# Kernel tuning notes

Hardware: AMD Instinct MI355X
Metric: run time of the kernel (lower is better)

Reference implementation:

```python
import jax, jax.numpy as jnp
import numpy as np

B, NPG, DEG = 128, 400, 16
N, E = B * NPG, B * NPG * DEG
E_PER = E // B
K1, K2, K3 = 360, 324, 292  # ceil(0.9*400), ceil(0.9*360), ceil(0.9*324)
EPS = 1e-5


def setup_inputs() -> dict:
    key = jax.random.key(0)
    ks = jax.random.split(key, 48)
    # edges constrained within each graph (contiguous equal-size graphs)
    g = jnp.repeat(jnp.arange(B, dtype=jnp.int32), E_PER)
    src = jax.random.randint(ks[0], (E,), 0, NPG, dtype=jnp.int32) + g * NPG
    dst = jax.random.randint(ks[1], (E,), 0, NPG, dtype=jnp.int32) + g * NPG
    inp = {
        'x': jax.random.normal(ks[2], (N, 64), dtype=jnp.float32),
        'edge_index': jnp.stack([src, dst]),
        'batch': jnp.repeat(jnp.arange(B, dtype=jnp.int32), NPG),
    }
    def glorot(k, a, b):
        lim = float(np.sqrt(6.0 / (a + b)))
        return jax.random.uniform(k, (a, b), minval=-lim, maxval=lim, dtype=jnp.float32)
    conv_dims = [(64, 32), (32, 64), (64, 128), (128, 128)]
    for i, (a, b) in enumerate(conv_dims, 1):
        inp[f'W{i}'] = glorot(ks[2 + i], a, b)
        inp[f'b{i}'] = jnp.zeros((b,), jnp.float32)
    for i, d in zip((1, 2, 3), (32, 64, 128)):
        inp[f'p{i}'] = jax.random.uniform(ks[8 + i], (d,), minval=-1.0, maxval=1.0, dtype=jnp.float32) / float(np.sqrt(d))
    lin_dims = [(128, 64), (64, 64), (64, 32), (32, 16), (16, 1)]
    for i, (a, b) in enumerate(lin_dims, 1):
        inp[f'Lw{i}'] = glorot(ks[12 + i], a, b)
        inp[f'Lb{i}'] = jnp.zeros((b,), jnp.float32)
    for i, d in enumerate((64, 64, 32, 16), 1):
        inp[f'g{i}'] = jnp.ones((d,), jnp.float32)
        inp[f'be{i}'] = jnp.zeros((d,), jnp.float32)
    return inp


def _gcn(x, src, dst, emask, nmask, W, b):
    h = x @ W
    deg = nmask + jax.ops.segment_sum(emask, dst, num_segments=N)
    dinv = jnp.where(deg > 0, jax.lax.rsqrt(deg), 0.0)
    norm = dinv[src] * dinv[dst] * emask
    agg = jax.ops.segment_sum(h[src] * norm[:, None], dst, num_segments=N)
    agg = agg + h * (dinv * dinv * nmask)[:, None]  # self-loop term
    return (agg + b) * nmask[:, None]


def _topk_pool(x, nmask, p, k):
    # PyG TopKPooling: score = x.p/||p||, keep top-k per graph, x *= tanh(score)
    score = (x @ p) / jnp.linalg.norm(p)
    sel = jnp.where(nmask > 0, score, -jnp.inf).reshape(B, NPG)
    _, idx = jax.lax.top_k(sel, k)
    gidx = (idx + (jnp.arange(B) * NPG)[:, None]).reshape(-1)
    new_mask = jnp.zeros((N,), x.dtype).at[gidx].set(1.0)
    return x * (jnp.tanh(score) * new_mask)[:, None], new_mask


def reference(x, edge_index, batch, W1, b1, p1, W2, b2, p2, W3, b3, p3, W4, b4,
              Lw1, Lb1, Lw2, Lb2, Lw3, Lb3, Lw4, Lb4, Lw5, Lb5,
              g1, be1, g2, be2, g3, be3, g4, be4):
    src, dst = edge_index[0], edge_index[1]
    nmask = jnp.ones((N,), jnp.float32)
    emask = jnp.ones((E,), jnp.float32)
    x = jax.nn.relu(_gcn(x, src, dst, emask, nmask, W1, b1))
    x, nmask = _topk_pool(x, nmask, p1, K1)
    emask = emask * nmask[src] * nmask[dst]
    x = jax.nn.relu(_gcn(x, src, dst, emask, nmask, W2, b2))
    x, nmask = _topk_pool(x, nmask, p2, K2)
    emask = emask * nmask[src] * nmask[dst]
    x = jax.nn.relu(_gcn(x, src, dst, emask, nmask, W3, b3))
    x, nmask = _topk_pool(x, nmask, p3, K3)
    emask = emask * nmask[src] * nmask[dst]
    x = jax.nn.relu(_gcn(x, src, dst, emask, nmask, W4, b4))
    h = x.reshape(B, NPG, -1).max(axis=1)
    def lin_bn(h, W, bb, ga, be):
        h = h @ W + bb
        m = h.mean(0)
        v = h.var(0)  # biased, matches BatchNorm1d training normalization
        return jax.nn.relu(ga * (h - m) / jnp.sqrt(v + EPS) + be)
    h = lin_bn(h, Lw1, Lb1, g1, be1)
    h = lin_bn(h, Lw2, Lb2, g2, be2)
    h = lin_bn(h, Lw3, Lb3, g3, be3)
    h = lin_bn(h, Lw4, Lb4, g4, be4)
    return h @ Lw5 + Lb5
```

## Files before the change

kernel.cpp:

```cpp
#include <hip/hip_runtime.h>
#include <math.h>

#define NNODES 51200
#define BGRAPHS 128
#define NPG 400
#define NEDGES 819200
#define EPG 6400
#define SLP 7680

__device__ __forceinline__ float4 ld4(const float* p) { return *reinterpret_cast<const float4*>(p); }
__device__ __forceinline__ void st4(float* p, float4 v) { *reinterpret_cast<float4*>(p) = v; }

__global__ __launch_bounds__(512) void csr_build_kernel(
    const int* __restrict__ src, const int* __restrict__ dst,
    unsigned short* __restrict__ slg, int* __restrict__ gsg, int* __restrict__ gcg,
    float* __restrict__ nmask, float* __restrict__ dinv, float* __restrict__ sc,
    float* __restrict__ hp) {
    __shared__ int deg[NPG];
    __shared__ int incl[512];
    __shared__ int gs[NPG];
    __shared__ int cur[NPG];
    const int g = blockIdx.x, t = threadIdx.x;
    for (int i = t; i < NPG; i += 512) deg[i] = 0;
    if (t < 128) hp[g * 128 + t] = 0.0f;
    __syncthreads();
    for (int e = t; e < EPG; e += 512)
        atomicAdd(&deg[dst[g * EPG + e] - g * NPG], 1);
    __syncthreads();
    const int d = (t < NPG) ? deg[t] : 0;
    const int p = (d + 3) >> 2;
    incl[t] = p;
    __syncthreads();
    for (int off = 1; off < 512; off <<= 1) {
        int add = (t >= off) ? incl[t - off] : 0;
        __syncthreads();
        incl[t] += add;
        __syncthreads();
    }
    if (t < NPG) {
        const int gstart = incl[t] - p;
        gs[t] = gstart;
        gsg[g * NPG + t] = gstart;
        gcg[g * NPG + t] = p;
        cur[t] = gstart * 4;
        nmask[g * NPG + t] = 1.0f;
        const float dv = rsqrtf(1.0f + (float)d);
        dinv[g * NPG + t] = dv;
        sc[g * NPG + t] = dv;
    }
    __syncthreads();
    for (int e = t; e < EPG; e += 512) {
        int dl = dst[g * EPG + e] - g * NPG;
        int pos = atomicAdd(&cur[dl], 1);
        slg[g * SLP + pos] = (unsigned short)(src[g * EPG + e] - g * NPG);
    }
    __syncthreads();
    if (t < NPG) {
        const int end = (gs[t] + p) * 4;
        for (int i = cur[t]; i < end; i++) slg[g * SLP + i] = (unsigned short)NPG;
    }
}

template<int IN, int OUT, int MODE>
__global__ __launch_bounds__(256) void gemm_kernel(
    const float* __restrict__ X, const float* __restrict__ W,
    const float* __restrict__ bias, const float* __restrict__ nmask,
    float* __restrict__ H, const float* __restrict__ p,
    float* __restrict__ score, float* __restrict__ hp) {
    __shared__ __align__(16) float sX[64 * IN];
    __shared__ unsigned smax[256];
    const int row0 = blockIdx.x * 64;
    const int t = threadIdx.x;
    for (int i = t; i < 64 * IN / 4; i += 256)
        reinterpret_cast<float4*>(sX)[i] =
            reinterpret_cast<const float4*>(X + (size_t)row0 * IN)[i];
    if (MODE == 3) smax[t] = 0u;
    __syncthreads();
    constexpr int CG  = OUT / 4;
    constexpr int RG  = 256 / CG;
    constexpr int RPT = 64 / RG;
    const int c0 = (t % CG) * 4;
    const int r0 = (t / CG) * RPT;
    float acc[RPT][4];
#pragma unroll
    for (int r = 0; r < RPT; r++)
#pragma unroll
        for (int j = 0; j < 4; j++) acc[r][j] = 0.0f;
    for (int k4 = 0; k4 < IN / 4; k4++) {
        const float4 w0 = ld4(&W[(k4 * 4 + 0) * OUT + c0]);
        const float4 w1 = ld4(&W[(k4 * 4 + 1) * OUT + c0]);
        const float4 w2 = ld4(&W[(k4 * 4 + 2) * OUT + c0]);
        const float4 w3 = ld4(&W[(k4 * 4 + 3) * OUT + c0]);
#pragma unroll
        for (int r = 0; r < RPT; r++) {
            const float4 xv = ld4(&sX[(r0 + r) * IN + k4 * 4]);
            acc[r][0] += xv.x * w0.x + xv.y * w1.x + xv.z * w2.x + xv.w * w3.x;
            acc[r][1] += xv.x * w0.y + xv.y * w1.y + xv.z * w2.y + xv.w * w3.y;
            acc[r][2] += xv.x * w0.z + xv.y * w1.z + xv.z * w2.z + xv.w * w3.z;
            acc[r][3] += xv.x * w0.w + xv.y * w1.w + xv.z * w2.w + xv.w * w3.w;
        }
    }
    const int graph0 = row0 / 400;
    const int bnd = (graph0 + 1) * 400;
    float ps[RPT];
    float cmax[4] = {0.f, 0.f, 0.f, 0.f};
#pragma unroll
    for (int r = 0; r < RPT; r++) {
        const int row = row0 + r0 + r;
        float4 v = make_float4(acc[r][0], acc[r][1], acc[r][2], acc[r][3]);
        if (MODE >= 2) {
            const float4 b4 = ld4(&bias[c0]);
            const float m = nmask[row];
            v.x = fmaxf(v.x + b4.x, 0.0f) * m;
            v.y = fmaxf(v.y + b4.y, 0.0f) * m;
            v.z = fmaxf(v.z + b4.z, 0.0f) * m;
            v.w = fmaxf(v.w + b4.w, 0.0f) * m;
        }
        if (MODE != 3) st4(&H[(size_t)row * OUT + c0], v);
        if (MODE == 2) {
            const float4 p4 = ld4(&p[c0]);
            ps[r] = v.x * p4.x + v.y * p4.y + v.z * p4.z + v.w * p4.w;
        }
        if (MODE == 3) {
            cmax[0] = fmaxf(cmax[0], v.x);
            cmax[1] = fmaxf(cmax[1], v.y);
            cmax[2] = fmaxf(cmax[2], v.z);
            cmax[3] = fmaxf(cmax[3], v.w);
        }
    }
    if (MODE == 2) {
#pragma unroll
        for (int r = 0; r < RPT; r++) {
#pragma unroll
            for (int off = 1; off < CG; off <<= 1) ps[r] += __shfl_xor(ps[r], off);
        }
        if ((t % CG) == 0) {
#pragma unroll
            for (int r = 0; r < RPT; r++) score[row0 + r0 + r] = ps[r];
        }
    }
    if (MODE == 3) {
        const int seg = ((row0 + r0) >= bnd) ? 1 : 0;
        atomicMax(&smax[seg * 128 + c0 + 0], __float_as_uint(cmax[0]));
        atomicMax(&smax[seg * 128 + c0 + 1], __float_as_uint(cmax[1]));
        atomicMax(&smax[seg * 128 + c0 + 2], __float_as_uint(cmax[2]));
        atomicMax(&smax[seg * 128 + c0 + 3], __float_as_uint(cmax[3]));
        __syncthreads();
        unsigned* hpu = reinterpret_cast<unsigned*>(hp);
        if (t < 128) atomicMax(&hpu[graph0 * 128 + t], smax[t]);
        const int graph1 = (row0 + 63) / 400;
        if (graph1 != graph0 && t < 128) atomicMax(&hpu[graph1 * 128 + t], smax[128 + t]);
    }
}

template<int OUT, int NCH, int NS, bool EPI, bool SCORE, bool TOPK>
__global__ __launch_bounds__(512) void gcn_agg_kernel(
    const float* __restrict__ H, float* __restrict__ Y,
    const float* __restrict__ dinv_g, const float* __restrict__ sc_g,
    const float* __restrict__ bias,
    const float* __restrict__ p_sc, float* __restrict__ score_out,
    const float* __restrict__ scoreb_in, const float* __restrict__ nmask_in,
    float* __restrict__ nmask_out, const float* __restrict__ p_pool,
    int K, int PDIM,
    const unsigned short* __restrict__ slg, const int* __restrict__ gsg,
    const int* __restrict__ gcg) {
    __shared__ __align__(16) float Hl[(NPG + 1) * 36];
    __shared__ float dinvl[NPG];
    __shared__ float scl[NPG];
    __shared__ int gsl[NPG];
    __shared__ int gcl[NPG];
    __shared__ unsigned long long sl64[SLP / 4];
    __shared__ float misc[4];
    const unsigned short* sl = reinterpret_cast<const unsigned short*>(sl64);
    const int b   = blockIdx.x;
    const int g   = b / (NCH * NS);
    const int rem = b % (NCH * NS);
    const int f0  = (rem / NS) * 32;
    const int n0  = (rem % NS) * (NPG / NS);
    const int t   = threadIdx.x;

    for (int i = t; i < NPG; i += 512) {
        gsl[i] = gsg[g * NPG + i];
        gcl[i] = gcg[g * NPG + i];
    }
    for (int i = t; i < SLP / 4; i += 512)
        sl64[i] = reinterpret_cast<const unsigned long long*>(slg + (size_t)g * SLP)[i];

    if (TOPK) {
        float* sval = Hl;
        int*   sidx = (int*)(Hl + 512);
        float* sraw = Hl + 1024;
        float* nml  = Hl + 1440;
        if (t < 64) {
            float s = 0.0f;
            for (int j = t; j < PDIM; j += 64) s += p_pool[j] * p_pool[j];
#pragma unroll
            for (int o = 32; o > 0; o >>= 1) s += __shfl_xor(s, o, 64);
            if (t == 0) misc[0] = sqrtf(s);
        }
        float v = -INFINITY;
        int ix = t;
        if (t < NPG) {
            const float raw = scoreb_in[g * NPG + t];
            sraw[t] = raw;
            v = (nmask_in[g * NPG + t] > 0.0f) ? raw : -INFINITY;
        }
        __syncthreads();
        for (int kk = 2; kk <= 512; kk <<= 1) {
            for (int j = kk >> 1; j > 0; j >>= 1) {
                float vb; int ib;
                if (j >= 64) {
                    sval[t] = v; sidx[t] = ix;
                    __syncthreads();
                    vb = sval[t ^ j]; ib = sidx[t ^ j];
                    __syncthreads();
                } else {
                    vb = __shfl_xor(v, j, 64);
                    ib = __shfl_xor(ix, j, 64);
                }
                const bool ownFirst = (v > vb) || (v == vb && ix < ib);
                const bool lower = (t & j) == 0;
                const bool desc = (t & kk) == 0;
                const bool keepOwn = lower ? (desc == ownFirst) : (desc != ownFirst);
                if (!keepOwn) { v = vb; ix = ib; }
            }
        }
        if (t <= NPG) nml[t] = 0.0f;
        __syncthreads();
        if (t < K) nml[ix] = 1.0f;
        __syncthreads();
        if (rem == 0 && t < NPG) nmask_out[g * NPG + t] = nml[t];
        const float spn = misc[0];
        for (int n = t; n < NPG; n += 512) {
            float dv = 0.0f;
            if (nml[n] > 0.0f) {
                float d = 1.0f;
                const int g0 = gsl[n], g1 = g0 + gcl[n];
                for (int gg = g0; gg < g1; ++gg) {
                    const unsigned long long q = *reinterpret_cast<const unsigned long long*>(&sl[gg * 4]);
                    d += nml[(int)(q & 0xFFFF)] + nml[(int)((q >> 16) & 0xFFFF)] +
                         nml[(int)((q >> 32) & 0xFFFF)] + nml[(int)(q >> 48)];
                }
                dv = rsqrtf(d);
            }
            dinvl[n] = dv;
            scl[n] = (nml[n] > 0.0f) ? tanhf(sraw[n] / spn) * dv : 0.0f;
        }
        __syncthreads();
    } else {
        for (int i = t; i < NPG; i += 512) {
            dinvl[i] = dinv_g[g * NPG + i];
            scl[i]   = sc_g[g * NPG + i];
        }
        __syncthreads();
    }

    for (int i = t; i < NPG * 8; i += 512) {
        const int n = i >> 3, q = i & 7;
        const float s = scl[n];
        float4 v = ld4(&H[(size_t)(g * NPG + n) * OUT + f0 + q * 4]);
        v.x *= s; v.y *= s; v.z *= s; v.w *= s;
        st4(&Hl[n * 36 + q * 4], v);
    }
    if (t < 36) Hl[NPG * 36 + t] = 0.0f;
    __syncthreads();

    const int wave = t >> 6, lane = t & 63;
    const int sub = lane >> 3, f4 = lane & 7;
    constexpr int NPB = NPG / NS;
    for (int n = n0 + wave * 8 + sub; n < n0 + NPB; n += 64) {
        const float di = dinvl[n];
        if (di == 0.0f) continue;
        const int g0 = gsl[n], g1 = g0 + gcl[n];
        float4 acc = ld4(&Hl[n * 36 + f4 * 4]);
        for (int gg = g0; gg < g1; ++gg) {
            const unsigned long long q = *reinterpret_cast<const unsigned long long*>(&sl[gg * 4]);
            const int s0 = (int)(q & 0xFFFF), s1 = (int)((q >> 16) & 0xFFFF);
            const int s2 = (int)((q >> 32) & 0xFFFF), s3 = (int)(q >> 48);
            const float4 a = ld4(&Hl[s0 * 36 + f4 * 4]);
            const float4 bb = ld4(&Hl[s1 * 36 + f4 * 4]);
            const float4 c = ld4(&Hl[s2 * 36 + f4 * 4]);
            const float4 dd = ld4(&Hl[s3 * 36 + f4 * 4]);
            acc.x += (a.x + bb.x) + (c.x + dd.x);
            acc.y += (a.y + bb.y) + (c.y + dd.y);
            acc.z += (a.z + bb.z) + (c.z + dd.z);
            acc.w += (a.w + bb.w) + (c.w + dd.w);
        }
        acc.x *= di; acc.y *= di; acc.z *= di; acc.w *= di;
        if (EPI) {
            const float4 b4 = ld4(&bias[f0 + f4 * 4]);
            acc.x = fmaxf(acc.x + b4.x, 0.0f);
            acc.y = fmaxf(acc.y + b4.y, 0.0f);
            acc.z = fmaxf(acc.z + b4.z, 0.0f);
            acc.w = fmaxf(acc.w + b4.w, 0.0f);
        }
        st4(&Y[(size_t)(g * NPG + n) * OUT + f0 + f4 * 4], acc);
        if (SCORE) {
            const float4 p4 = ld4(&p_sc[f4 * 4]);
            float part = acc.x * p4.x + acc.y * p4.y + acc.z * p4.z + acc.w * p4.w;
            part += __shfl_xor(part, 1);
            part += __shfl_xor(part, 2);
            part += __shfl_xor(part, 4);
            if (f4 == 0) score_out[g * NPG + n] = part;
        }
    }
}

__global__ __launch_bounds__(512) void conv2_fused_kernel(
    const float* __restrict__ X0, float* __restrict__ X1,
    const float* __restrict__ scoreb_in, const float* __restrict__ nmask_in,
    float* __restrict__ nmask_out, float* __restrict__ scoreb_out,
    const float* __restrict__ p_pool,
    const float* __restrict__ W2, const float* __restrict__ b2,
    const float* __restrict__ p2,
    const unsigned short* __restrict__ slg, const int* __restrict__ gsg,
    const int* __restrict__ gcg) {
    __shared__ __align__(16) float Hl[(NPG + 1) * 36];
    __shared__ __align__(16) float out2[200 * 36];
    __shared__ float dinvl[NPG];
    __shared__ float scl[NPG];
    __shared__ int gsl[NPG];
    __shared__ int gcl[NPG];
    __shared__ unsigned long long sl64[SLP / 4];
    __shared__ float misc[4];
    const unsigned short* sl = reinterpret_cast<const unsigned short*>(sl64);
    const int b = blockIdx.x, g = b >> 1, seg = b & 1;
    const int n0 = seg * 200;
    const int t = threadIdx.x;

    for (int i = t; i < NPG; i += 512) {
        gsl[i] = gsg[g * NPG + i];
        gcl[i] = gcg[g * NPG + i];
    }
    for (int i = t; i < SLP / 4; i += 512)
        sl64[i] = reinterpret_cast<const unsigned long long*>(slg + (size_t)g * SLP)[i];

    {
        float* sval = Hl;
        int*   sidx = (int*)(Hl + 512);
        float* sraw = Hl + 1024;
        float* nml  = Hl + 1440;
        if (t < 64) {
            float s = 0.0f;
            for (int j = t; j < 32; j += 64) s += p_pool[j] * p_pool[j];
#pragma unroll
            for (int o = 32; o > 0; o >>= 1) s += __shfl_xor(s, o, 64);
            if (t == 0) misc[0] = sqrtf(s);
        }
        float v = -INFINITY;
        int ix = t;
        if (t < NPG) {
            const float raw = scoreb_in[g * NPG + t];
            sraw[t] = raw;
            v = (nmask_in[g * NPG + t] > 0.0f) ? raw : -INFINITY;
        }
        __syncthreads();
        for (int kk = 2; kk <= 512; kk <<= 1) {
            for (int j = kk >> 1; j > 0; j >>= 1) {
                float vb; int ib;
                if (j >= 64) {
                    sval[t] = v; sidx[t] = ix;
                    __syncthreads();
                    vb = sval[t ^ j]; ib = sidx[t ^ j];
                    __syncthreads();
                } else {
                    vb = __shfl_xor(v, j, 64);
                    ib = __shfl_xor(ix, j, 64);
                }
                const bool ownFirst = (v > vb) || (v == vb && ix < ib);
                const bool lower = (t & j) == 0;
                const bool desc = (t & kk) == 0;
                const bool keepOwn = lower ? (desc == ownFirst) : (desc != ownFirst);
                if (!keepOwn) { v = vb; ix = ib; }
            }
        }
        if (t <= NPG) nml[t] = 0.0f;
        __syncthreads();
        if (t < 360) nml[ix] = 1.0f;
        __syncthreads();
        if (seg == 0 && t < NPG) nmask_out[g * NPG + t] = nml[t];
        const float spn = misc[0];
        for (int n = t; n < NPG; n += 512) {
            float dv = 0.0f;
            if (nml[n] > 0.0f) {
                float d = 1.0f;
                const int g0 = gsl[n], g1 = g0 + gcl[n];
                for (int gg = g0; gg < g1; ++gg) {
                    const unsigned long long q = *reinterpret_cast<const unsigned long long*>(&sl[gg * 4]);
                    d += nml[(int)(q & 0xFFFF)] + nml[(int)((q >> 16) & 0xFFFF)] +
                         nml[(int)((q >> 32) & 0xFFFF)] + nml[(int)(q >> 48)];
                }
                dv = rsqrtf(d);
            }
            dinvl[n] = dv;
            scl[n] = (nml[n] > 0.0f) ? tanhf(sraw[n] / spn) * dv : 0.0f;
        }
        __syncthreads();
    }

    for (int i = t; i < NPG * 8; i += 512) {
        const int n = i >> 3, q = i & 7;
        const float s = scl[n];
        float4 v = ld4(&X0[(size_t)(g * NPG + n) * 32 + q * 4]);
        v.x *= s; v.y *= s; v.z *= s; v.w *= s;
        st4(&Hl[n * 36 + q * 4], v);
    }
    if (t < 36) Hl[NPG * 36 + t] = 0.0f;
    __syncthreads();

    {
        const int wave = t >> 6, lane = t & 63;
        const int sub = lane >> 3, f4 = lane & 7;
        for (int n = n0 + wave * 8 + sub; n < n0 + 200; n += 64) {
            const float di = dinvl[n];
            float4 acc = make_float4(0.f, 0.f, 0.f, 0.f);
            if (di != 0.0f) {
                acc = ld4(&Hl[n * 36 + f4 * 4]);
                const int g0 = gsl[n], g1 = g0 + gcl[n];
                for (int gg = g0; gg < g1; ++gg) {
                    const unsigned long long q = *reinterpret_cast<const unsigned long long*>(&sl[gg * 4]);
                    const int s0 = (int)(q & 0xFFFF), s1 = (int)((q >> 16) & 0xFFFF);
                    const int s2 = (int)((q >> 32) & 0xFFFF), s3 = (int)(q >> 48);
                    const float4 a = ld4(&Hl[s0 * 36 + f4 * 4]);
                    const float4 bb = ld4(&Hl[s1 * 36 + f4 * 4]);
                    const float4 c = ld4(&Hl[s2 * 36 + f4 * 4]);
                    const float4 dd = ld4(&Hl[s3 * 36 + f4 * 4]);
                    acc.x += (a.x + bb.x) + (c.x + dd.x);
                    acc.y += (a.y + bb.y) + (c.y + dd.y);
                    acc.z += (a.z + bb.z) + (c.z + dd.z);
                    acc.w += (a.w + bb.w) + (c.w + dd.w);
                }
                acc.x *= di; acc.y *= di; acc.z *= di; acc.w *= di;
            }
            st4(&out2[(n - n0) * 36 + f4 * 4], acc);
        }
    }
    __syncthreads();

    {
        const int c0 = (t & 15) * 4;
        const int slot = t >> 4;
        for (int n = n0 + slot; n < n0 + 200; n += 32) {
            float a0 = 0.f, a1 = 0.f, a2 = 0.f, a3 = 0.f;
            for (int k4 = 0; k4 < 8; k4++) {
                const float4 w0 = ld4(&W2[(k4 * 4 + 0) * 64 + c0]);
                const float4 w1 = ld4(&W2[(k4 * 4 + 1) * 64 + c0]);
                const float4 w2 = ld4(&W2[(k4 * 4 + 2) * 64 + c0]);
                const float4 w3 = ld4(&W2[(k4 * 4 + 3) * 64 + c0]);
                const float4 xv = ld4(&out2[(n - n0) * 36 + k4 * 4]);
                a0 += xv.x * w0.x + xv.y * w1.x + xv.z * w2.x + xv.w * w3.x;
                a1 += xv.x * w0.y + xv.y * w1.y + xv.z * w2.y + xv.w * w3.y;
                a2 += xv.x * w0.z + xv.y * w1.z + xv.z * w2.z + xv.w * w3.z;
                a3 += xv.x * w0.w + xv.y * w1.w + xv.z * w2.w + xv.w * w3.w;
            }
            const float m = (dinvl[n] > 0.0f) ? 1.0f : 0.0f;
            const float4 bb = ld4(&b2[c0]);
            float4 v = make_float4(fmaxf(a0 + bb.x, 0.f) * m, fmaxf(a1 + bb.y, 0.f) * m,
                                   fmaxf(a2 + bb.z, 0.f) * m, fmaxf(a3 + bb.w, 0.f) * m);
            st4(&X1[(size_t)(g * NPG + n) * 64 + c0], v);
            const float4 p4 = ld4(&p2[c0]);
            float ps = v.x * p4.x + v.y * p4.y + v.z * p4.z + v.w * p4.w;
            ps += __shfl_xor(ps, 1); ps += __shfl_xor(ps, 2);
            ps += __shfl_xor(ps, 4); ps += __shfl_xor(ps, 8);
            if ((t & 15) == 0) scoreb_out[g * NPG + n] = ps;
        }
    }
}

template<int IN, int OUT>
__global__ __launch_bounds__(128) void head_layer_kernel(
    const float* __restrict__ A, const float* __restrict__ W,
    const float* __restrict__ b, const float* __restrict__ ga,
    const float* __restrict__ be, float* __restrict__ Y) {
    __shared__ float Al[128 * (IN + 1)];
    __shared__ float red[4];
    const int c = blockIdx.x, t = threadIdx.x;
    for (int i = t; i < 128 * IN; i += 128)
        Al[(i / IN) * (IN + 1) + (i % IN)] = A[i];
    __syncthreads();
    float acc = b[c];
#pragma unroll
    for (int j = 0; j < IN; j++) acc += Al[t * (IN + 1) + j] * W[j * OUT + c];
    float s1 = acc, s2 = acc * acc;
    for (int o = 32; o > 0; o >>= 1) {
        s1 += __shfl_down(s1, o, 64);
        s2 += __shfl_down(s2, o, 64);
    }
    if ((t & 63) == 0) { red[t >> 6] = s1; red[2 + (t >> 6)] = s2; }
    __syncthreads();
    const float S1 = red[0] + red[1], S2 = red[2] + red[3];
    const float m = S1 * (1.0f / 128.0f);
    const float var = S2 * (1.0f / 128.0f) - m * m;
    float val = ga[c] * (acc - m) * rsqrtf(var + 1e-5f) + be[c];
    Y[t * OUT + c] = fmaxf(val, 0.0f);
}

__global__ __launch_bounds__(512) void head_tail_kernel(
    const float* __restrict__ A2,
    const float* __restrict__ Lw3, const float* __restrict__ Lb3,
    const float* __restrict__ g3, const float* __restrict__ be3,
    const float* __restrict__ Lw4, const float* __restrict__ Lb4,
    const float* __restrict__ g4, const float* __restrict__ be4,
    const float* __restrict__ Lw5, const float* __restrict__ Lb5,
    float* __restrict__ out) {
    __shared__ __align__(16) float A[128 * 68];
    __shared__ __align__(16) float Z[128 * 36];
    __shared__ __align__(16) float Z2[128 * 20];
    __shared__ float mv[64];
    const int t = threadIdx.x;
    for (int i = t; i < 128 * 16; i += 512) {
        const int r = i >> 4, q = i & 15;
        st4(&A[r * 68 + q * 4], ld4(&A2[r * 64 + q * 4]));
    }
    __syncthreads();
    {
        const int c = t & 31, rs = t >> 5;
        for (int r = rs; r < 128; r += 16) {
            float acc = Lb3[c];
            for (int j4 = 0; j4 < 16; j4++) {
                const float4 a = ld4(&A[r * 68 + j4 * 4]);
                acc += a.x * Lw3[(j4 * 4 + 0) * 32 + c] + a.y * Lw3[(j4 * 4 + 1) * 32 + c]
                     + a.z * Lw3[(j4 * 4 + 2) * 32 + c] + a.w * Lw3[(j4 * 4 + 3) * 32 + c];
            }
            Z[r * 36 + c] = acc;
        }
    }
    __syncthreads();
    if (t < 32) {
        float s1 = 0.f, s2 = 0.f;
        for (int r = 0; r < 128; r++) { const float v = Z[r * 36 + t]; s1 += v; s2 += v * v; }
        const float m = s1 * (1.0f / 128.0f);
        mv[t] = m; mv[32 + t] = s2 * (1.0f / 128.0f) - m * m;
    }
    __syncthreads();
    {
        const int c = t & 31;
        const float m = mv[c], scn = g3[c] * rsqrtf(mv[32 + c] + 1e-5f), bb = be3[c];
        for (int r = t >> 5; r < 128; r += 16)
            Z[r * 36 + c] = fmaxf((Z[r * 36 + c] - m) * scn + bb, 0.f);
    }
    __syncthreads();
    {
        const int c = t & 15, rs = t >> 4;
        for (int r = rs; r < 128; r += 32) {
            float acc = Lb4[c];
            for (int j4 = 0; j4 < 8; j4++) {
                const float4 a = ld4(&Z[r * 36 + j4 * 4]);
                acc += a.x * Lw4[(j4 * 4 + 0) * 16 + c] + a.y * Lw4[(j4 * 4 + 1) * 16 + c]
                     + a.z * Lw4[(j4 * 4 + 2) * 16 + c] + a.w * Lw4[(j4 * 4 + 3) * 16 + c];
            }
            Z2[r * 20 + c] = acc;
        }
    }
    __syncthreads();
    if (t < 16) {
        float s1 = 0.f, s2 = 0.f;
        for (int r = 0; r < 128; r++) { const float v = Z2[r * 20 + t]; s1 += v; s2 += v * v; }
        const float m = s1 * (1.0f / 128.0f);
        mv[t] = m; mv[32 + t] = s2 * (1.0f / 128.0f) - m * m;
    }
    __syncthreads();
    if (t < 128) {
        float acc = Lb5[0];
#pragma unroll
        for (int j = 0; j < 16; j++) {
            const float v = fmaxf((Z2[t * 20 + j] - mv[j]) * (g4[j] * rsqrtf(mv[32 + j] + 1e-5f)) + be4[j], 0.f);
            acc += v * Lw5[j];
        }
        out[t] = acc;
    }
}

extern "C" void kernel_launch(void* const* d_in, const int* in_sizes, int n_in,
                              void* d_out, int out_size, void* d_ws, size_t ws_size,
                              hipStream_t stream) {
    (void)in_sizes; (void)n_in; (void)out_size; (void)ws_size;
    const float* x   = (const float*)d_in[0];
    const int*   ei  = (const int*)d_in[1];
    const float* W1  = (const float*)d_in[3];  const float* b1  = (const float*)d_in[4];
    const float* W2  = (const float*)d_in[5];  const float* b2  = (const float*)d_in[6];
    const float* W3  = (const float*)d_in[7];  const float* b3  = (const float*)d_in[8];
    const float* W4  = (const float*)d_in[9];  const float* b4  = (const float*)d_in[10];
    const float* p1  = (const float*)d_in[11];
    const float* p2  = (const float*)d_in[12];
    const float* p3  = (const float*)d_in[13];
    const float* Lw1 = (const float*)d_in[14]; const float* Lb1 = (const float*)d_in[15];
    const float* Lw2 = (const float*)d_in[16]; const float* Lb2 = (const float*)d_in[17];
    const float* Lw3 = (const float*)d_in[18]; const float* Lb3 = (const float*)d_in[19];
    const float* Lw4 = (const float*)d_in[20]; const float* Lb4 = (const float*)d_in[21];
    const float* Lw5 = (const float*)d_in[22]; const float* Lb5 = (const float*)d_in[23];
    const float* g1  = (const float*)d_in[24]; const float* be1 = (const float*)d_in[25];
    const float* g2  = (const float*)d_in[26]; const float* be2 = (const float*)d_in[27];
    const float* g3  = (const float*)d_in[28]; const float* be3 = (const float*)d_in[29];
    const float* g4  = (const float*)d_in[30]; const float* be4 = (const float*)d_in[31];

    const int* src = ei;
    const int* dst = ei + NEDGES;

    float* ws    = (float*)d_ws;
    float* hb    = ws;
    float* x0    = hb + (size_t)NNODES * 128;
    float* x1    = x0 + (size_t)NNODES * 128;
    float* nmA   = x1 + (size_t)NNODES * 128;
    float* nmB   = nmA + NNODES;
    float* dinv  = nmB + NNODES;
    float* sc    = dinv + NNODES;
    float* scbA  = sc + NNODES;
    float* scbB  = scbA + NNODES;
    float* hp    = scbB + NNODES;
    float* a1    = hp + 128 * 128;
    float* a2    = a1 + 128 * 64;
    unsigned short* slg = (unsigned short*)(a2 + 128 * 64);
    int* gsg = (int*)(slg + (size_t)BGRAPHS * SLP);
    int* gcg = gsg + (size_t)BGRAPHS * NPG;

    csr_build_kernel<<<BGRAPHS, 512, 0, stream>>>(src, dst, slg, gsg, gcg, nmA, dinv, sc, hp);

    gemm_kernel<64, 32, 0><<<NNODES / 64, 256, 0, stream>>>(x, W1, nullptr, nullptr, hb, nullptr, nullptr, nullptr);
    gcn_agg_kernel<32, 1, 2, true, true, false><<<BGRAPHS * 2, 512, 0, stream>>>(
        hb, x0, dinv, sc, b1, p1, scbA,
        nullptr, nullptr, nullptr, nullptr, 0, 0, slg, gsg, gcg);

    conv2_fused_kernel<<<BGRAPHS * 2, 512, 0, stream>>>(
        x0, x1, scbA, nmA, nmB, scbB, p1, W2, b2, p2, slg, gsg, gcg);

    gcn_agg_kernel<64, 2, 2, false, false, true><<<BGRAPHS * 4, 512, 0, stream>>>(
        x1, hb, nullptr, nullptr, nullptr, nullptr, nullptr,
        scbB, nmB, nmA, p2, 324, 64, slg, gsg, gcg);
    gemm_kernel<64, 128, 2><<<NNODES / 64, 256, 0, stream>>>(hb, W3, b3, nmA, x0, p3, scbA, nullptr);

    gcn_agg_kernel<128, 4, 1, false, false, true><<<BGRAPHS * 4, 512, 0, stream>>>(
        x0, hb, nullptr, nullptr, nullptr, nullptr, nullptr,
        scbA, nmA, nmB, p3, 292, 128, slg, gsg, gcg);
    gemm_kernel<128, 128, 3><<<NNODES / 64, 256, 0, stream>>>(hb, W4, b4, nmB, x1, nullptr, nullptr, hp);

    head_layer_kernel<128, 64><<<64, 128, 0, stream>>>(hp, Lw1, Lb1, g1, be1, a1);
    head_layer_kernel<64, 64><<<64, 128, 0, stream>>>(a1, Lw2, Lb2, g2, be2, a2);
    head_tail_kernel<<<1, 512, 0, stream>>>(a2, Lw3, Lb3, g3, be3, Lw4, Lb4, g4, be4, Lw5, Lb5, (float*)d_out);
}
```

Baseline: 192.4 us.

## Fuse CSR build and first GEMM into one heterogeneous kernel launch

The CSR construction kernel and the first 64->32 projection GEMM are merged into one launch. The first 128 blocks build per-graph adjacency and the remaining 256 blocks run the GEMM over 128-row tiles, so the two independent phases run concurrently and one launch is dropped. Because MODE 0 is no longer used, the gemm template's bias/relu/mask epilogue is made unconditional. The cost is a larger shared allocation for every block and an uneven block workload.

```diff
diff --git a/kernel.cpp b/kernel.cpp
--- a/kernel.cpp
+++ b/kernel.cpp
@@ -11,53 +11,94 @@
 __device__ __forceinline__ float4 ld4(const float* p) { return *reinterpret_cast<const float4*>(p); }
 __device__ __forceinline__ void st4(float* p, float4 v) { *reinterpret_cast<float4*>(p) = v; }
 
-__global__ __launch_bounds__(512) void csr_build_kernel(
+__global__ __launch_bounds__(512) void csr_gemm1_kernel(
     const int* __restrict__ src, const int* __restrict__ dst,
     unsigned short* __restrict__ slg, int* __restrict__ gsg, int* __restrict__ gcg,
     float* __restrict__ nmask, float* __restrict__ dinv, float* __restrict__ sc,
-    float* __restrict__ hp) {
-    __shared__ int deg[NPG];
-    __shared__ int incl[512];
-    __shared__ int gs[NPG];
-    __shared__ int cur[NPG];
-    const int g = blockIdx.x, t = threadIdx.x;
-    for (int i = t; i < NPG; i += 512) deg[i] = 0;
-    if (t < 128) hp[g * 128 + t] = 0.0f;
-    __syncthreads();
-    for (int e = t; e < EPG; e += 512)
-        atomicAdd(&deg[dst[g * EPG + e] - g * NPG], 1);
-    __syncthreads();
-    const int d = (t < NPG) ? deg[t] : 0;
-    const int p = (d + 3) >> 2;
-    incl[t] = p;
-    __syncthreads();
-    for (int off = 1; off < 512; off <<= 1) {
-        int add = (t >= off) ? incl[t - off] : 0;
-        __syncthreads();
-        incl[t] += add;
-        __syncthreads();
-    }
-    if (t < NPG) {
-        const int gstart = incl[t] - p;
-        gs[t] = gstart;
-        gsg[g * NPG + t] = gstart;
-        gcg[g * NPG + t] = p;
-        cur[t] = gstart * 4;
-        nmask[g * NPG + t] = 1.0f;
-        const float dv = rsqrtf(1.0f + (float)d);
-        dinv[g * NPG + t] = dv;
-        sc[g * NPG + t] = dv;
-    }
-    __syncthreads();
-    for (int e = t; e < EPG; e += 512) {
-        int dl = dst[g * EPG + e] - g * NPG;
-        int pos = atomicAdd(&cur[dl], 1);
-        slg[g * SLP + pos] = (unsigned short)(src[g * EPG + e] - g * NPG);
-    }
-    __syncthreads();
-    if (t < NPG) {
-        const int end = (gs[t] + p) * 4;
-        for (int i = cur[t]; i < end; i++) slg[g * SLP + i] = (unsigned short)NPG;
+    float* __restrict__ hp,
+    const float* __restrict__ x, const float* __restrict__ W1, float* __restrict__ hb) {
+    __shared__ __align__(16) char smem[128 * 64 * 4];
+    const int t = threadIdx.x;
+    if (blockIdx.x < BGRAPHS) {
+        int* deg  = (int*)smem;
+        int* incl = deg + 512;
+        int* gs   = incl + 512;
+        int* cur  = gs + NPG;
+        const int g = blockIdx.x;
+        for (int i = t; i < NPG; i += 512) deg[i] = 0;
+        if (t < 128) hp[g * 128 + t] = 0.0f;
+        __syncthreads();
+        for (int e = t; e < EPG; e += 512)
+            atomicAdd(&deg[dst[g * EPG + e] - g * NPG], 1);
+        __syncthreads();
+        const int d = (t < NPG) ? deg[t] : 0;
+        const int p = (d + 3) >> 2;
+        incl[t] = p;
+        __syncthreads();
+        for (int off = 1; off < 512; off <<= 1) {
+            int add = (t >= off) ? incl[t - off] : 0;
+            __syncthreads();
+            incl[t] += add;
+            __syncthreads();
+        }
+        if (t < NPG) {
+            const int gstart = incl[t] - p;
+            gs[t] = gstart;
+            gsg[g * NPG + t] = gstart;
+            gcg[g * NPG + t] = p;
+            cur[t] = gstart * 4;
+            nmask[g * NPG + t] = 1.0f;
+            const float dv = rsqrtf(1.0f + (float)d);
+            dinv[g * NPG + t] = dv;
+            sc[g * NPG + t] = dv;
+        }
+        __syncthreads();
+        for (int e = t; e < EPG; e += 512) {
+            int dl = dst[g * EPG + e] - g * NPG;
+            int pos = atomicAdd(&cur[dl], 1);
+            slg[g * SLP + pos] = (unsigned short)(src[g * EPG + e] - g * NPG);
+        }
+        __syncthreads();
+        if (t < NPG) {
+            const int end = (gs[t] + p) * 4;
+            for (int i = cur[t]; i < end; i++) slg[g * SLP + i] = (unsigned short)NPG;
+        }
+    } else {
+        float* sX = (float*)smem;
+        const int bid2 = blockIdx.x - BGRAPHS;
+        const int c0 = (t & 7) * 4;
+        const int rg = t >> 3;
+        for (int tile = bid2; tile < 400; tile += 256) {
+            const int row0 = tile * 128;
+            __syncthreads();
+            for (int i = t; i < 128 * 64 / 4; i += 512)
+                reinterpret_cast<float4*>(sX)[i] =
+                    reinterpret_cast<const float4*>(x + (size_t)row0 * 64)[i];
+            __syncthreads();
+            float acc[2][4];
+#pragma unroll
+            for (int r = 0; r < 2; r++)
+#pragma unroll
+                for (int j = 0; j < 4; j++) acc[r][j] = 0.0f;
+            for (int k4 = 0; k4 < 16; k4++) {
+                const float4 w0 = ld4(&W1[(k4 * 4 + 0) * 32 + c0]);
+                const float4 w1 = ld4(&W1[(k4 * 4 + 1) * 32 + c0]);
+                const float4 w2 = ld4(&W1[(k4 * 4 + 2) * 32 + c0]);
+                const float4 w3 = ld4(&W1[(k4 * 4 + 3) * 32 + c0]);
+#pragma unroll
+                for (int r = 0; r < 2; r++) {
+                    const float4 xv = ld4(&sX[(rg * 2 + r) * 64 + k4 * 4]);
+                    acc[r][0] += xv.x * w0.x + xv.y * w1.x + xv.z * w2.x + xv.w * w3.x;
+                    acc[r][1] += xv.x * w0.y + xv.y * w1.y + xv.z * w2.y + xv.w * w3.y;
+                    acc[r][2] += xv.x * w0.z + xv.y * w1.z + xv.z * w2.z + xv.w * w3.z;
+                    acc[r][3] += xv.x * w0.w + xv.y * w1.w + xv.z * w2.w + xv.w * w3.w;
+                }
+            }
+#pragma unroll
+            for (int r = 0; r < 2; r++)
+                st4(&hb[(size_t)(row0 + rg * 2 + r) * 32 + c0],
+                    make_float4(acc[r][0], acc[r][1], acc[r][2], acc[r][3]));
+        }
     }
 }
 
@@ -108,14 +149,12 @@
     for (int r = 0; r < RPT; r++) {
         const int row = row0 + r0 + r;
         float4 v = make_float4(acc[r][0], acc[r][1], acc[r][2], acc[r][3]);
-        if (MODE >= 2) {
-            const float4 b4 = ld4(&bias[c0]);
-            const float m = nmask[row];
-            v.x = fmaxf(v.x + b4.x, 0.0f) * m;
-            v.y = fmaxf(v.y + b4.y, 0.0f) * m;
-            v.z = fmaxf(v.z + b4.z, 0.0f) * m;
-            v.w = fmaxf(v.w + b4.w, 0.0f) * m;
-        }
+        const float4 b4 = ld4(&bias[c0]);
+        const float m = nmask[row];
+        v.x = fmaxf(v.x + b4.x, 0.0f) * m;
+        v.y = fmaxf(v.y + b4.y, 0.0f) * m;
+        v.z = fmaxf(v.z + b4.z, 0.0f) * m;
+        v.w = fmaxf(v.w + b4.w, 0.0f) * m;
         if (MODE != 3) st4(&H[(size_t)row * OUT + c0], v);
         if (MODE == 2) {
             const float4 p4 = ld4(&p[c0]);
@@ -614,9 +653,9 @@
     int* gsg = (int*)(slg + (size_t)BGRAPHS * SLP);
     int* gcg = gsg + (size_t)BGRAPHS * NPG;
 
-    csr_build_kernel<<<BGRAPHS, 512, 0, stream>>>(src, dst, slg, gsg, gcg, nmA, dinv, sc, hp);
-
-    gemm_kernel<64, 32, 0><<<NNODES / 64, 256, 0, stream>>>(x, W1, nullptr, nullptr, hb, nullptr, nullptr, nullptr);
+    csr_gemm1_kernel<<<BGRAPHS + 256, 512, 0, stream>>>(
+        src, dst, slg, gsg, gcg, nmA, dinv, sc, hp, x, W1, hb);
+
     gcn_agg_kernel<32, 1, 2, true, true, false><<<BGRAPHS * 2, 512, 0, stream>>>(
         hb, x0, dinv, sc, b1, p1, scbA,
         nullptr, nullptr, nullptr, nullptr, 0, 0, slg, gsg, gcg);
```

New measurement: 252.3 us. 31.1% more time.
